# Optimization experiments

Measured on AMD Instinct MI355X. Metric: run time of the kernel, lower is better.

The kernel has to match this reference:

```python
import jax, jax.numpy as jnp
import numpy as np

B, S, D, H, HD, FFN_MULT = 4, 2048, 2048, 16, 128, 4
EPS = 1e-8


def setup_inputs() -> dict:
    key = jax.random.key(0)
    ks = jax.random.split(key, 12)
    s = lambda k, shape, scale: (jax.random.normal(k, shape, dtype=jnp.float32) * scale)
    d_ff = D * FFN_MULT
    return {
        "x": s(ks[0], (B, S, D), 1.0),
        # per-head Q/K/V projections, stacked: [H, D, HD] (no bias, as in source)
        "wq": s(ks[1], (H, D, HD), D ** -0.5),
        "wk": s(ks[2], (H, D, HD), D ** -0.5),
        "wv": s(ks[3], (H, D, HD), D ** -0.5),
        # output projection Linear(D, D) with bias
        "wo": s(ks[4], (D, D), D ** -0.5),
        "bo": jnp.zeros((D,), jnp.float32),
        # FFN: Linear(D, d_ff) -> ReLU -> Linear(d_ff, D), both with bias
        "w1": s(ks[5], (D, d_ff), D ** -0.5),
        "b1": jnp.zeros((d_ff,), jnp.float32),
        "w2": s(ks[6], (d_ff, D), d_ff ** -0.5),
        "b2": jnp.zeros((D,), jnp.float32),
        # RMSNorm gains
        "g1": jnp.ones((D,), jnp.float32),
        "g2": jnp.ones((D,), jnp.float32),
    }


def rms_norm(x, g):
    return x * jax.lax.rsqrt(jnp.mean(x * x, axis=-1, keepdims=True) + EPS) * g


def attention(h, wq, wk, wv, wo, bo):
    # per-head projections batched over heads: [B,S,D] x [H,D,K] -> [B,H,S,K]
    q = jnp.einsum("bsd,hdk->bhsk", h, wq)
    k = jnp.einsum("bsd,hdk->bhsk", h, wk)
    v = jnp.einsum("bsd,hdk->bhsk", h, wv)
    scores = jnp.einsum("bhsk,bhtk->bhst", q, k) * (HD ** -0.5)
    causal = jnp.tril(jnp.ones((S, S), dtype=bool))
    scores = jnp.where(causal, scores, -jnp.inf)
    attn = jax.nn.softmax(scores, axis=-1)
    out = jnp.einsum("bhst,bhtk->bhsk", attn, v)  # [B,H,S,HD]
    # concat heads along feature dim (head order matches torch.cat over heads)
    out = out.transpose(0, 2, 1, 3).reshape(B, S, D)
    return out @ wo + bo


def reference(x, wq, wk, wv, wo, bo, w1, b1, w2, b2, g1, g2):
    x = x + attention(rms_norm(x, g1), wq, wk, wv, wo, bo)
    h = rms_norm(x, g2)
    ffn = jax.nn.relu(h @ w1 + b1) @ w2 + b2
    return x + ffn
```

## Files before the change

kernel.cpp:

```cpp
#include <hip/hip_runtime.h>
#include <hip/hip_bf16.h>

#define Bsz 4
#define Ssz 2048
#define Dsz 2048
#define Hn 16
#define HDsz 128
#define DFF 8192
#define Msz (Bsz*Ssz)

typedef __bf16 bf16x8 __attribute__((ext_vector_type(8)));
typedef float  f32x4  __attribute__((ext_vector_type(4)));

enum { FLAG_BIAS=1, FLAG_RELU=2, FLAG_RESID=4, FLAG_F32OUT=8, FLAG_QKV=16 };

#define GLDS16(g, l) __builtin_amdgcn_global_load_lds( \
    (const __attribute__((address_space(1))) unsigned int*)(g), \
    (__attribute__((address_space(3))) unsigned int*)(l), 16, 0, 0)

#define SBAR       asm volatile("s_barrier" ::: "memory")
#define WAIT_VM3   asm volatile("s_waitcnt vmcnt(3)" ::: "memory")
#define WAIT_VM0   asm volatile("s_waitcnt vmcnt(0)" ::: "memory")

template <typename TIN>
__global__ __launch_bounds__(256) void transpose_cvt(
    const TIN* __restrict__ in, __bf16* __restrict__ out,
    int R, int C, long long inRS, int subB,
    long long strideOuter, long long strideInner, long long outBS)
{
  __shared__ float tile[32][33];
  int bz = blockIdx.z;
  const TIN* inp = in + (size_t)(bz / subB) * strideOuter + (size_t)(bz % subB) * strideInner;
  __bf16* outp = out + (size_t)bz * outBS;
  int tx = threadIdx.x, ty = threadIdx.y;
  int c  = blockIdx.x * 32 + tx;
  int r0 = blockIdx.y * 32;
#pragma unroll
  for (int i = 0; i < 4; ++i) {
    int r = r0 + ty + i * 8;
    tile[ty + i * 8][tx] = (float)inp[(size_t)r * inRS + c];
  }
  __syncthreads();
  int oc  = r0 + tx;
  int or0 = blockIdx.x * 32;
#pragma unroll
  for (int i = 0; i < 4; ++i) {
    int orr = or0 + ty + i * 8;
    outp[(size_t)orr * R + oc] = (__bf16)tile[tx][ty + i * 8];
  }
}

__global__ __launch_bounds__(256) void rmsnorm_k(
    const float* __restrict__ x, const float* __restrict__ g, __bf16* __restrict__ out)
{
  int row = blockIdx.x, tid = threadIdx.x;
  const float4* xr = (const float4*)(x + (size_t)row * Dsz);
  float4 v0 = xr[tid*2], v1 = xr[tid*2+1];
  float ss = v0.x*v0.x + v0.y*v0.y + v0.z*v0.z + v0.w*v0.w
           + v1.x*v1.x + v1.y*v1.y + v1.z*v1.z + v1.w*v1.w;
#pragma unroll
  for (int off = 32; off > 0; off >>= 1) ss += __shfl_down(ss, off);
  __shared__ float wsum[4];
  __shared__ float sc;
  if ((tid & 63) == 0) wsum[tid >> 6] = ss;
  __syncthreads();
  if (tid == 0) {
    float t = wsum[0] + wsum[1] + wsum[2] + wsum[3];
    sc = rsqrtf(t * (1.0f / (float)Dsz) + 1e-8f);
  }
  __syncthreads();
  float s = sc;
  const float4* gr = (const float4*)g;
  float4 g0 = gr[tid*2], g1v = gr[tid*2+1];
  bf16x8 ov;
  ov[0]=(__bf16)(v0.x*s*g0.x);  ov[1]=(__bf16)(v0.y*s*g0.y);
  ov[2]=(__bf16)(v0.z*s*g0.z);  ov[3]=(__bf16)(v0.w*s*g0.w);
  ov[4]=(__bf16)(v1.x*s*g1v.x); ov[5]=(__bf16)(v1.y*s*g1v.y);
  ov[6]=(__bf16)(v1.z*s*g1v.z); ov[7]=(__bf16)(v1.w*s*g1v.w);
  *(bf16x8*)(out + (size_t)row * Dsz + tid * 8) = ov;
}

#define WSTG(Xb, Xlds, buf, kh, kst) \
    GLDS16((Xb) + (size_t)wrloc * K + (kst) + (kh)*32 + wsloc, (Xlds) + (buf)*32768 + (kh)*16384 + wwuni)
#define WLDA(kh, mi) (*(const bf16x8*)(AsB + cur*32768 + (kh)*16384 + (wr*64 + (mi)*16 + l15)*64 + psl))
#define WLDB(kh, nj) (*(const bf16x8*)(BsB + cur*32768 + (kh)*16384 + (wc*64 + (nj)*16 + l15)*64 + psl))

__global__ __launch_bounds__(1024) void gemm_w(
    const __bf16* __restrict__ A, const __bf16* __restrict__ B,
    const float* __restrict__ bias, const float* __restrict__ resid,
    void* __restrict__ Cout, void* __restrict__ CoutV,
    int M, int N, int K, int flags)
{
  __shared__ __align__(16) __bf16 As[2*2*256*32];
  __shared__ __align__(16) __bf16 Bs[2*2*256*32];
  int nwg = gridDim.x;
  int id = blockIdx.x;
  id = (id & 7) * (nwg >> 3) + (id >> 3);
  int ntn = N >> 8;
  int tm = id / ntn, tn = id - tm * ntn;
  int tid = threadIdx.x;
  int lane = tid & 63, w = tid >> 6;
  int l15 = lane & 15, lg = lane >> 4;
  int wr = w >> 2, wc = w & 3;
  const __bf16* Ab = A + (size_t)tm * 256 * K;
  const __bf16* Bb = B + (size_t)tn * 256 * K;
  char* AsB = (char*)As;
  char* BsB = (char*)Bs;
  int wrloc = tid >> 2;
  int wsloc = ((lane & 3) ^ ((lane >> 3) & 3)) * 8;
  int wwuni = w * 1024;
  int psl  = (lg ^ ((l15 >> 1) & 3)) * 16;
  f32x4 zero; zero[0]=0.f; zero[1]=0.f; zero[2]=0.f; zero[3]=0.f;
  f32x4 acc[4][4];
#pragma unroll
  for (int i = 0; i < 4; ++i)
#pragma unroll
    for (int j = 0; j < 4; ++j) acc[i][j] = zero;
  int NT = K >> 6;
  WSTG(Ab, AsB, 0, 0, 0);
  WSTG(Ab, AsB, 0, 1, 0);
  WSTG(Bb, BsB, 0, 0, 0);
  WSTG(Bb, BsB, 0, 1, 0);
  WAIT_VM0; SBAR;
  int cur = 0;
  for (int t = 0; t < NT; ++t) {
    int nb = cur ^ 1;
    int kst = (t + 1 < NT) ? ((t + 1) << 6) : 0;
    WSTG(Ab, AsB, nb, 0, kst);
    WSTG(Ab, AsB, nb, 1, kst);
    WSTG(Bb, BsB, nb, 0, kst);
    WSTG(Bb, BsB, nb, 1, kst);
    {
      bf16x8 af[4], bf[4];
      af[0]=WLDA(0,0); af[1]=WLDA(0,1); af[2]=WLDA(0,2); af[3]=WLDA(0,3);
      bf[0]=WLDB(0,0); bf[1]=WLDB(0,1); bf[2]=WLDB(0,2); bf[3]=WLDB(0,3);
#pragma unroll
      for (int mi = 0; mi < 4; ++mi)
#pragma unroll
        for (int nj = 0; nj < 4; ++nj)
          acc[mi][nj] = __builtin_amdgcn_mfma_f32_16x16x32_bf16(af[mi], bf[nj], acc[mi][nj], 0, 0, 0);
    }
    {
      bf16x8 af[4], bf[4];
      af[0]=WLDA(1,0); af[1]=WLDA(1,1); af[2]=WLDA(1,2); af[3]=WLDA(1,3);
      bf[0]=WLDB(1,0); bf[1]=WLDB(1,1); bf[2]=WLDB(1,2); bf[3]=WLDB(1,3);
#pragma unroll
      for (int mi = 0; mi < 4; ++mi)
#pragma unroll
        for (int nj = 0; nj < 4; ++nj)
          acc[mi][nj] = __builtin_amdgcn_mfma_f32_16x16x32_bf16(af[mi], bf[nj], acc[mi][nj], 0, 0, 0);
    }
    WAIT_VM0;
    SBAR;
    cur = nb;
  }
  int cm = tm * 256 + wr * 64;
  int cn = tn * 256 + wc * 64;
  float*  Cf = (float*)Cout;
  __bf16* Cb;
  int Ns = N, cnb = cn;
  if (flags & FLAG_QKV) {
    int which = cn >> 11;
    Cb = (which == 2) ? (__bf16*)CoutV
                      : ((__bf16*)Cout + (size_t)which * Msz * 2048);
    Ns = 2048; cnb = cn & 2047;
  } else {
    Cb = (__bf16*)Cout;
  }
#pragma unroll
  for (int m = 0; m < 4; ++m) {
#pragma unroll
    for (int nj = 0; nj < 4; ++nj) {
      int col  = cn  + nj * 16 + l15;
      int colo = cnb + nj * 16 + l15;
      float bv = (flags & FLAG_BIAS) ? bias[col] : 0.0f;
#pragma unroll
      for (int r = 0; r < 4; ++r) {
        int row = cm + m * 16 + 4 * lg + r;
        float v = acc[m][nj][r] + bv;
        if (flags & FLAG_RELU) v = v > 0.f ? v : 0.f;
        size_t idx = (size_t)row * Ns + colo;
        if (flags & FLAG_RESID) v += resid[idx];
        if (flags & FLAG_F32OUT) Cf[idx] = v;
        else                     Cb[idx] = (__bf16)v;
      }
    }
  }
}

#define NSTGA(buf, kst) do { \
    GLDS16(Ab + (size_t)(rloc      ) * K + (kst) + sloc, AsB + (buf)*16384 +        wuni); \
    GLDS16(Ab + (size_t)(rloc + 128) * K + (kst) + sloc, AsB + (buf)*16384 + 8192 + wuni); \
  } while (0)
#define NSTGB(buf, kst) \
    GLDS16(Bb + (size_t)rloc * K + (kst) + sloc, BsB + (buf)*8192 + wuni)
#define NLDA(mi) (*(const bf16x8*)(AsB + cur*16384 + (wr*64 + (mi)*16 + l15)*64 + psl))
#define NLDB(nj) (*(const bf16x8*)(BsB + cur*8192  + (wc*64 + (nj)*16 + l15)*64 + psl))

__global__ __launch_bounds__(512, 4) void gemm_n(
    const __bf16* __restrict__ A, const __bf16* __restrict__ B,
    const float* __restrict__ bias, const float* __restrict__ resid,
    void* __restrict__ Cout, void* __restrict__ CoutV,
    int M, int N, int K, int flags)
{
  __shared__ __align__(16) __bf16 As[3*256*32];
  __shared__ __align__(16) __bf16 Bs[3*128*32];
  int nwg = gridDim.x;
  int id = blockIdx.x;
  id = (id & 7) * (nwg >> 3) + (id >> 3);
  int ntn = N >> 7;
  int tm = id / ntn, tn = id - tm * ntn;
  int tid = threadIdx.x;
  int lane = tid & 63, w = tid >> 6;
  int l15 = lane & 15, lg = lane >> 4;
  int wr = w >> 1, wc = w & 1;
  const __bf16* Ab = A + (size_t)tm * 256 * K;
  const __bf16* Bb = B + (size_t)tn * 128 * K;
  char* AsB = (char*)As;
  char* BsB = (char*)Bs;
  int rloc = tid >> 2;
  int sloc = ((lane & 3) ^ ((lane >> 3) & 3)) * 8;
  int wuni = w * 1024;
  int psl  = (lg ^ ((l15 >> 1) & 3)) * 16;
  f32x4 zero; zero[0]=0.f; zero[1]=0.f; zero[2]=0.f; zero[3]=0.f;
  f32x4 acc[4][4];
#pragma unroll
  for (int i = 0; i < 4; ++i)
#pragma unroll
    for (int j = 0; j < 4; ++j) acc[i][j] = zero;
  int NT = K >> 5;
  NSTGA(0, 0);  NSTGB(0, 0);
  NSTGA(1, 32); NSTGB(1, 32);
  WAIT_VM3; SBAR;
  int cur = 0;
  for (int t = 0; t < NT; ++t) {
    int sb = cur + 2; if (sb >= 3) sb -= 3;
    int kst = (t + 2 < NT) ? ((t + 2) << 5) : 0;
    NSTGA(sb, kst);
    NSTGB(sb, kst);
    bf16x8 af[4], bf[4];
    af[0]=NLDA(0); af[1]=NLDA(1); af[2]=NLDA(2); af[3]=NLDA(3);
    bf[0]=NLDB(0); bf[1]=NLDB(1); bf[2]=NLDB(2); bf[3]=NLDB(3);
#pragma unroll
    for (int mi = 0; mi < 4; ++mi)
#pragma unroll
      for (int nj = 0; nj < 4; ++nj)
        acc[mi][nj] = __builtin_amdgcn_mfma_f32_16x16x32_bf16(af[mi], bf[nj], acc[mi][nj], 0, 0, 0);
    WAIT_VM3;
    SBAR;
    cur += 1; if (cur >= 3) cur -= 3;
  }
  WAIT_VM0;
  int cm = tm * 256 + wr * 64;
  int cn = tn * 128 + wc * 64;
  float*  Cf = (float*)Cout;
  __bf16* Cb;
  int Ns = N, cnb = cn;
  if (flags & FLAG_QKV) {
    int which = cn >> 11;
    Cb = (which == 2) ? (__bf16*)CoutV
                      : ((__bf16*)Cout + (size_t)which * Msz * 2048);
    Ns = 2048; cnb = cn & 2047;
  } else {
    Cb = (__bf16*)Cout;
  }
#pragma unroll
  for (int m = 0; m < 4; ++m) {
#pragma unroll
    for (int nj = 0; nj < 4; ++nj) {
      int col  = cn  + nj * 16 + l15;
      int colo = cnb + nj * 16 + l15;
      float bv = (flags & FLAG_BIAS) ? bias[col] : 0.0f;
#pragma unroll
      for (int r = 0; r < 4; ++r) {
        int row = cm + m * 16 + 4 * lg + r;
        float v = acc[m][nj][r] + bv;
        if (flags & FLAG_RELU) v = v > 0.f ? v : 0.f;
        size_t idx = (size_t)row * Ns + colo;
        if (flags & FLAG_RESID) v += resid[idx];
        if (flags & FLAG_F32OUT) Cf[idx] = v;
        else                     Cb[idx] = (__bf16)v;
      }
    }
  }
}

__global__ __launch_bounds__(512) void fattn(
    const __bf16* __restrict__ q, const __bf16* __restrict__ k,
    const __bf16* __restrict__ vt, __bf16* __restrict__ o)
{
  __shared__ __align__(16) __bf16 Ks[64*128];
  __shared__ __align__(16) __bf16 Vs[144*64];
  __shared__ __align__(16) __bf16 Ps[8][16*72];
  int bx = blockIdx.x, bh = blockIdx.y;
  int b = bh >> 4, h = bh & 15;
  int tid = threadIdx.x, lane = tid & 63, w = tid >> 6;
  int l15 = lane & 15, lg = lane >> 4;
  size_t base = ((size_t)b * Ssz) * Dsz + (size_t)h * HDsz;
  size_t vtb  = (size_t)bh * HDsz * Ssz;
  const float scale = 0.08838834764831845f;
  char* KsB = (char*)Ks;
  char* VsB = (char*)Vs;
  f32x4 zero; zero[0]=0.f; zero[1]=0.f; zero[2]=0.f; zero[3]=0.f;
  int ktr[2], khc[2], vhd[2], vtc[2];
#pragma unroll
  for (int j = 0; j < 2; ++j) {
    int c = tid + j * 512;
    ktr[j] = c >> 4;  khc[j] = (c & 15) ^ (ktr[j] & 7);
    vhd[j] = c >> 3;  vtc[j] = (c & 7) ^ (vhd[j] & 7);
  }
  int wuni = (tid & ~63) * 16;
  {
    int idx = tid * 2;
    int rr = 128 + (idx >> 6), cc = idx & 63;
    __bf16 v1 = (rr == 128) ? (__bf16)1.0f : (__bf16)0.0f;
    *(__bf16*)(VsB + rr * 128 + cc * 2)     = v1;
    *(__bf16*)(VsB + rr * 128 + cc * 2 + 2) = v1;
  }

  for (int ph = 0; ph < 2; ++ph) {
    int qt = ph ? bx : (15 - bx);
    int qs = qt * 128;
    int qmin = qs + w * 16;
    bf16x8 qf[4];
    int qrow = qmin + l15;
#pragma unroll
    for (int kk = 0; kk < 4; ++kk)
      qf[kk] = *(const bf16x8*)(q + base + (size_t)qrow * Dsz + kk * 32 + lg * 8);
    f32x4 acc[9];
#pragma unroll
    for (int i = 0; i < 9; ++i) acc[i] = zero;
    float mr[4];
#pragma unroll
    for (int r = 0; r < 4; ++r) mr[r] = -1e30f;
    int NT = 2 * qt + 2;
    for (int kt = 0; kt < NT; ++kt) {
      int t0 = kt * 64;
#pragma unroll
      for (int j = 0; j < 2; ++j) {
        GLDS16(k  + base + (size_t)(t0 + ktr[j]) * Dsz + khc[j] * 8,
               KsB + j * 8192 + wuni);
        GLDS16(vt + vtb  + (size_t)vhd[j] * Ssz + t0 + vtc[j] * 8,
               VsB + j * 8192 + wuni);
      }
      __syncthreads();
      bool act = (t0 <= qmin + 15);
      if (act) {
        f32x4 s[4];
#pragma unroll
        for (int cg = 0; cg < 4; ++cg) s[cg] = zero;
        __builtin_amdgcn_s_setprio(1);
#pragma unroll
        for (int kk = 0; kk < 4; ++kk) {
#pragma unroll
          for (int cg = 0; cg < 4; ++cg) {
            int tl = cg * 16 + l15;
            bf16x8 kf = *(const bf16x8*)(KsB + ((tl * 256 + kk * 64 + lg * 16) ^ ((tl & 7) << 4)));
            s[cg] = __builtin_amdgcn_mfma_f32_16x16x32_bf16(qf[kk], kf, s[cg], 0, 0, 0);
          }
        }
        __builtin_amdgcn_s_setprio(0);
        bool nm = (t0 + 63 > qmin);
        float rm[4];
        bool sk = true;
#pragma unroll
        for (int r = 0; r < 4; ++r) {
          int qr = qmin + 4 * lg + r;
          float m0 = -1e30f;
#pragma unroll
          for (int cg = 0; cg < 4; ++cg) {
            float sv = s[cg][r] * scale;
            if (nm && (t0 + cg * 16 + l15) > qr) sv = -1e30f;
            s[cg][r] = sv;
            m0 = fmaxf(m0, sv);
          }
          m0 = fmaxf(m0, __shfl_xor(m0, 1));
          m0 = fmaxf(m0, __shfl_xor(m0, 2));
          m0 = fmaxf(m0, __shfl_xor(m0, 4));
          m0 = fmaxf(m0, __shfl_xor(m0, 8));
          rm[r] = m0;
          sk = sk && (m0 <= mr[r] + 8.0f);
        }
        if (!__all(sk)) {
          f32x4 av;
#pragma unroll
          for (int r = 0; r < 4; ++r) {
            float mn = fmaxf(mr[r], rm[r]);
            av[r] = __expf(mr[r] - mn);
            mr[r] = mn;
          }
#pragma unroll
          for (int hg = 0; hg < 9; ++hg) acc[hg] *= av;
        }
#pragma unroll
        for (int r = 0; r < 4; ++r)
#pragma unroll
          for (int cg = 0; cg < 4; ++cg)
            Ps[w][(4 * lg + r) * 72 + cg * 16 + l15] = (__bf16)__expf(s[cg][r] - mr[r]);
        __builtin_amdgcn_s_setprio(1);
#pragma unroll
        for (int tt = 0; tt < 2; ++tt) {
          bf16x8 pf = *(const bf16x8*)((char*)&Ps[w][0] + l15 * 144 + tt * 64 + lg * 16);
#pragma unroll
          for (int hg = 0; hg < 9; ++hg) {
            int hd = hg * 16 + l15;
            bf16x8 vf = *(const bf16x8*)(VsB + ((hd * 128 + tt * 64 + lg * 16) ^ ((hd & 7) << 4)));
            acc[hg] = __builtin_amdgcn_mfma_f32_16x16x32_bf16(pf, vf, acc[hg], 0, 0, 0);
          }
        }
        __builtin_amdgcn_s_setprio(0);
      }
      __syncthreads();
    }
    f32x4 inv;
#pragma unroll
    for (int r = 0; r < 4; ++r)
      inv[r] = 1.0f / __shfl(acc[8][r], lane & 48);
#pragma unroll
    for (int hg = 0; hg < 8; ++hg) {
      f32x4 ov = acc[hg] * inv;
#pragma unroll
      for (int r = 0; r < 4; ++r) {
        int qr2 = qmin + 4 * lg + r;
        o[base + (size_t)qr2 * Dsz + hg * 16 + l15] = (__bf16)ov[r];
      }
    }
  }
}

extern "C" void kernel_launch(void* const* d_in, const int* in_sizes, int n_in,
                              void* d_out, int out_size, void* d_ws, size_t ws_size,
                              hipStream_t stream)
{
  (void)in_sizes; (void)n_in; (void)out_size; (void)ws_size;
  const float* x  = (const float*)d_in[0];
  const float* wq = (const float*)d_in[1];
  const float* wk = (const float*)d_in[2];
  const float* wv = (const float*)d_in[3];
  const float* wo = (const float*)d_in[4];
  const float* bo = (const float*)d_in[5];
  const float* w1 = (const float*)d_in[6];
  const float* b1 = (const float*)d_in[7];
  const float* w2 = (const float*)d_in[8];
  const float* b2 = (const float*)d_in[9];
  const float* g1 = (const float*)d_in[10];
  const float* g2 = (const float*)d_in[11];
  float* out = (float*)d_out;
  char* ws = (char*)d_ws;

  const size_t U = (size_t)2048 * 2048 * 2;
  __bf16* wqT = (__bf16*)(ws);
  __bf16* wkT = (__bf16*)(ws + U);
  __bf16* wvT = (__bf16*)(ws + 2*U);
  __bf16* woT = (__bf16*)(ws + 3*U);
  __bf16* w1T = (__bf16*)(ws + 4*U);
  __bf16* w2T = (__bf16*)(ws + 8*U);
  __bf16* h1  = (__bf16*)(ws + 12*U);
  __bf16* vb  = (__bf16*)(ws + 16*U);
  __bf16* vT    = h1;
  __bf16* attno = vb;
  __bf16* fb    = h1;
  __bf16* h2    = (__bf16*)(ws);
  __bf16* qb = (__bf16*)d_out;
  __bf16* kb = qb + (size_t)Msz * Dsz;
  float*  x2 = (float*)d_out;

  dim3 tb(32, 8, 1);
  transpose_cvt<float><<<dim3(4,64,16),  tb, 0, stream>>>(wq, wqT, 2048, 128, 128, 1, (long long)2048*128, 0, (long long)128*2048);
  transpose_cvt<float><<<dim3(4,64,16),  tb, 0, stream>>>(wk, wkT, 2048, 128, 128, 1, (long long)2048*128, 0, (long long)128*2048);
  transpose_cvt<float><<<dim3(4,64,16),  tb, 0, stream>>>(wv, wvT, 2048, 128, 128, 1, (long long)2048*128, 0, (long long)128*2048);
  transpose_cvt<float><<<dim3(64,64,1),  tb, 0, stream>>>(wo, woT, 2048, 2048, 2048, 1, 0, 0, 0);
  transpose_cvt<float><<<dim3(256,64,1), tb, 0, stream>>>(w1, w1T, 2048, 8192, 8192, 1, 0, 0, 0);
  transpose_cvt<float><<<dim3(64,128,2), tb, 0, stream>>>(w2, w2T, 4096, 2048, 2048, 1, (long long)4096*2048, 0, (long long)2048*4096);
  rmsnorm_k<<<8192, 256, 0, stream>>>(x, g1, h1);
  gemm_w<<<768, 1024, 0, stream>>>(h1, wqT, nullptr, nullptr, qb, vb, Msz, 6144, 2048, FLAG_QKV);
  transpose_cvt<__bf16><<<dim3(4,64,64), tb, 0, stream>>>(vb, vT, 2048, 128, 2048, 16, (long long)2048*2048, 128, (long long)128*2048);
  fattn<<<dim3(8, 64), 512, 0, stream>>>(qb, kb, vT, attno);
  gemm_n<<<512, 512, 0, stream>>>(attno, woT, bo, x, x2, nullptr, Msz, 2048, 2048, FLAG_BIAS | FLAG_RESID | FLAG_F32OUT);
  rmsnorm_k<<<8192, 256, 0, stream>>>(x2, g2, h2);
  for (int c = 0; c < 2; ++c) {
    gemm_n<<<1024, 512, 0, stream>>>(h2, w1T + (size_t)c*4096*2048, b1 + c*4096, nullptr,
                                     fb, nullptr, Msz, 4096, 2048, FLAG_BIAS | FLAG_RELU);
    int fl = FLAG_RESID | FLAG_F32OUT | (c == 0 ? FLAG_BIAS : 0);
    gemm_n<<<512, 512, 0, stream>>>(fb, w2T + (size_t)c*2048*4096, b2, x2,
                                    out, nullptr, Msz, 2048, 4096, fl);
  }
}
```

Baseline: 1.258 ms.

## Restructure QKV GEMM into 4-stage K pipeline with 512 threads and larger warp tiles

The fused QKV projection GEMM now runs with 512 threads instead of 1024. Each warp computes a 128x64 output tile instead of 64x64, so every B fragment loaded from LDS feeds more MFMAs. The K loop steps by 32 through a 4-buffer ring in LDS, prefetching three stages ahead and using a partial vmcnt wait instead of fully draining each iteration. This hides global-load latency and cuts LDS reads per MFMA, at the cost of fewer waves per CU and higher accumulator register pressure.

Result: slower. 1.298 ms (+3.2%).

```diff
diff --git a/kernel.cpp b/kernel.cpp
--- a/kernel.cpp
+++ b/kernel.cpp
@@ -19,6 +19,7 @@
     (__attribute__((address_space(3))) unsigned int*)(l), 16, 0, 0)
 
 #define SBAR       asm volatile("s_barrier" ::: "memory")
+#define WAIT_VM8   asm volatile("s_waitcnt vmcnt(8)" ::: "memory")
 #define WAIT_VM3   asm volatile("s_waitcnt vmcnt(3)" ::: "memory")
 #define WAIT_VM0   asm volatile("s_waitcnt vmcnt(0)" ::: "memory")
 
@@ -80,19 +81,25 @@
   *(bf16x8*)(out + (size_t)row * Dsz + tid * 8) = ov;
 }
 
-#define WSTG(Xb, Xlds, buf, kh, kst) \
-    GLDS16((Xb) + (size_t)wrloc * K + (kst) + (kh)*32 + wsloc, (Xlds) + (buf)*32768 + (kh)*16384 + wwuni)
-#define WLDA(kh, mi) (*(const bf16x8*)(AsB + cur*32768 + (kh)*16384 + (wr*64 + (mi)*16 + l15)*64 + psl))
-#define WLDB(kh, nj) (*(const bf16x8*)(BsB + cur*32768 + (kh)*16384 + (wc*64 + (nj)*16 + l15)*64 + psl))
-
-__global__ __launch_bounds__(1024) void gemm_w(
+#define W2STGA(buf, kst) do { \
+    GLDS16(Ab + (size_t)(rloc      ) * K + (kst) + sloc, AsB + (buf)*16384 +        wuni); \
+    GLDS16(Ab + (size_t)(rloc + 128) * K + (kst) + sloc, AsB + (buf)*16384 + 8192 + wuni); \
+  } while (0)
+#define W2STGB(buf, kst) do { \
+    GLDS16(Bb + (size_t)(rloc      ) * K + (kst) + sloc, BsB + (buf)*16384 +        wuni); \
+    GLDS16(Bb + (size_t)(rloc + 128) * K + (kst) + sloc, BsB + (buf)*16384 + 8192 + wuni); \
+  } while (0)
+#define W2LDA(mi) (*(const bf16x8*)(AsB + cur*16384 + (wr*128 + (mi)*16 + l15)*64 + psl))
+#define W2LDB(nj) (*(const bf16x8*)(BsB + cur*16384 + (wc*64  + (nj)*16 + l15)*64 + psl))
+
+__global__ __launch_bounds__(512) void gemm_w(
     const __bf16* __restrict__ A, const __bf16* __restrict__ B,
     const float* __restrict__ bias, const float* __restrict__ resid,
     void* __restrict__ Cout, void* __restrict__ CoutV,
     int M, int N, int K, int flags)
 {
-  __shared__ __align__(16) __bf16 As[2*2*256*32];
-  __shared__ __align__(16) __bf16 Bs[2*2*256*32];
+  __shared__ __align__(16) __bf16 As[4*256*32];
+  __shared__ __align__(16) __bf16 Bs[4*256*32];
   int nwg = gridDim.x;
   int id = blockIdx.x;
   id = (id & 7) * (nwg >> 3) + (id >> 3);
@@ -106,55 +113,40 @@
   const __bf16* Bb = B + (size_t)tn * 256 * K;
   char* AsB = (char*)As;
   char* BsB = (char*)Bs;
-  int wrloc = tid >> 2;
-  int wsloc = ((lane & 3) ^ ((lane >> 3) & 3)) * 8;
-  int wwuni = w * 1024;
+  int rloc = tid >> 2;
+  int sloc = ((lane & 3) ^ ((lane >> 3) & 3)) * 8;
+  int wuni = w * 1024;
   int psl  = (lg ^ ((l15 >> 1) & 3)) * 16;
   f32x4 zero; zero[0]=0.f; zero[1]=0.f; zero[2]=0.f; zero[3]=0.f;
-  f32x4 acc[4][4];
-#pragma unroll
-  for (int i = 0; i < 4; ++i)
+  f32x4 acc[8][4];
+#pragma unroll
+  for (int i = 0; i < 8; ++i)
 #pragma unroll
     for (int j = 0; j < 4; ++j) acc[i][j] = zero;
-  int NT = K >> 6;
-  WSTG(Ab, AsB, 0, 0, 0);
-  WSTG(Ab, AsB, 0, 1, 0);
-  WSTG(Bb, BsB, 0, 0, 0);
-  WSTG(Bb, BsB, 0, 1, 0);
-  WAIT_VM0; SBAR;
-  int cur = 0;
+  int NT = K >> 5;
+  W2STGA(0, 0);  W2STGB(0, 0);
+  W2STGA(1, 32); W2STGB(1, 32);
+  W2STGA(2, 64); W2STGB(2, 64);
+  WAIT_VM8; SBAR;
   for (int t = 0; t < NT; ++t) {
-    int nb = cur ^ 1;
-    int kst = (t + 1 < NT) ? ((t + 1) << 6) : 0;
-    WSTG(Ab, AsB, nb, 0, kst);
-    WSTG(Ab, AsB, nb, 1, kst);
-    WSTG(Bb, BsB, nb, 0, kst);
-    WSTG(Bb, BsB, nb, 1, kst);
-    {
-      bf16x8 af[4], bf[4];
-      af[0]=WLDA(0,0); af[1]=WLDA(0,1); af[2]=WLDA(0,2); af[3]=WLDA(0,3);
-      bf[0]=WLDB(0,0); bf[1]=WLDB(0,1); bf[2]=WLDB(0,2); bf[3]=WLDB(0,3);
-#pragma unroll
-      for (int mi = 0; mi < 4; ++mi)
-#pragma unroll
-        for (int nj = 0; nj < 4; ++nj)
-          acc[mi][nj] = __builtin_amdgcn_mfma_f32_16x16x32_bf16(af[mi], bf[nj], acc[mi][nj], 0, 0, 0);
+    int cur = t & 3, sb = (t + 3) & 3;
+    int kst = (t + 3 < NT) ? ((t + 3) << 5) : 0;
+    W2STGA(sb, kst);
+    W2STGB(sb, kst);
+    bf16x8 bf[4];
+    bf[0]=W2LDB(0); bf[1]=W2LDB(1); bf[2]=W2LDB(2); bf[3]=W2LDB(3);
+#pragma unroll
+    for (int mi = 0; mi < 8; ++mi) {
+      bf16x8 af = W2LDA(mi);
+#pragma unroll
+      for (int nj = 0; nj < 4; ++nj)
+        acc[mi][nj] = __builtin_amdgcn_mfma_f32_16x16x32_bf16(af, bf[nj], acc[mi][nj], 0, 0, 0);
     }
-    {
-      bf16x8 af[4], bf[4];
-      af[0]=WLDA(1,0); af[1]=WLDA(1,1); af[2]=WLDA(1,2); af[3]=WLDA(1,3);
-      bf[0]=WLDB(1,0); bf[1]=WLDB(1,1); bf[2]=WLDB(1,2); bf[3]=WLDB(1,3);
-#pragma unroll
-      for (int mi = 0; mi < 4; ++mi)
-#pragma unroll
-        for (int nj = 0; nj < 4; ++nj)
-          acc[mi][nj] = __builtin_amdgcn_mfma_f32_16x16x32_bf16(af[mi], bf[nj], acc[mi][nj], 0, 0, 0);
-    }
-    WAIT_VM0;
+    WAIT_VM8;
     SBAR;
-    cur = nb;
-  }
-  int cm = tm * 256 + wr * 64;
+  }
+  WAIT_VM0;
+  int cm = tm * 256 + wr * 128;
   int cn = tn * 256 + wc * 64;
   float*  Cf = (float*)Cout;
   __bf16* Cb;
@@ -168,7 +160,7 @@
     Cb = (__bf16*)Cout;
   }
 #pragma unroll
-  for (int m = 0; m < 4; ++m) {
+  for (int m = 0; m < 8; ++m) {
 #pragma unroll
     for (int nj = 0; nj < 4; ++nj) {
       int col  = cn  + nj * 16 + l15;
@@ -473,7 +465,7 @@
   transpose_cvt<float><<<dim3(256,64,1), tb, 0, stream>>>(w1, w1T, 2048, 8192, 8192, 1, 0, 0, 0);
   transpose_cvt<float><<<dim3(64,128,2), tb, 0, stream>>>(w2, w2T, 4096, 2048, 2048, 1, (long long)4096*2048, 0, (long long)2048*4096);
   rmsnorm_k<<<8192, 256, 0, stream>>>(x, g1, h1);
-  gemm_w<<<768, 1024, 0, stream>>>(h1, wqT, nullptr, nullptr, qb, vb, Msz, 6144, 2048, FLAG_QKV);
+  gemm_w<<<768, 512, 0, stream>>>(h1, wqT, nullptr, nullptr, qb, vb, Msz, 6144, 2048, FLAG_QKV);
   transpose_cvt<__bf16><<<dim3(4,64,64), tb, 0, stream>>>(vb, vT, 2048, 128, 2048, 16, (long long)2048*2048, 128, (long long)128*2048);
   fattn<<<dim3(8, 64), 512, 0, stream>>>(qb, kb, vT, attno);
   gemm_n<<<512, 512, 0, stream>>>(attno, woT, bo, x, x2, nullptr, Msz, 2048, 2048, FLAG_BIAS | FLAG_RESID | FLAG_F32OUT);
```
